# Kernel optimization log

Hardware: AMD Instinct MI355X
Metric: run time of the kernel (lower is better)

Reference implementation:

```python
import jax, jax.numpy as jnp
import numpy as np

T, HID, H, HKV, D = 4096, 2048, 16, 2, 128
EPS = 1e-6


def setup_inputs() -> dict:
    key = jax.random.key(0)
    ks = jax.random.split(key, 5)
    hidden_states = jax.random.normal(ks[0], (T, HID), dtype=jnp.float32)
    # rope angles: build realistic cos/sin from positions and inv-freqs
    inv_freq = 1.0 / (10000.0 ** (jnp.arange(0, D, 2, dtype=jnp.float32) / D))
    ang = jnp.arange(T, dtype=jnp.float32)[:, None] * inv_freq[None, :]  # [T, D/2]
    ang = jnp.concatenate([ang, ang], axis=-1)  # [T, D]
    cos, sin = jnp.cos(ang), jnp.sin(ang)
    w_qkv = jax.random.normal(ks[1], (HID, (2 * H + 2 * HKV) * D), dtype=jnp.float32) * (HID ** -0.5)
    w_o = jax.random.normal(ks[2], (H * D, HID), dtype=jnp.float32) * ((H * D) ** -0.5)
    q_norm_w = jnp.ones((D,), dtype=jnp.float32)
    k_norm_w = jnp.ones((D,), dtype=jnp.float32)
    return {"hidden_states": hidden_states, "cos": cos, "sin": sin,
            "w_qkv": w_qkv, "w_o": w_o, "q_norm_w": q_norm_w, "k_norm_w": k_norm_w}


def _rms_norm(x, w):
    var = jnp.mean(x * x, axis=-1, keepdims=True)
    return x * jax.lax.rsqrt(var + EPS) * w


def _rotate_half(x):
    x1, x2 = x[..., : D // 2], x[..., D // 2:]
    return jnp.concatenate([-x2, x1], axis=-1)


def _rope(x, cos, sin):
    # x: [T, h, D]; cos/sin: [T, D]
    return x * cos[:, None, :] + _rotate_half(x) * sin[:, None, :]


def reference(hidden_states, cos, sin, w_qkv, w_o, q_norm_w, k_norm_w):
    qkv = hidden_states @ w_qkv  # [T, (2H+2HKV)*D]
    q_sz, kv_sz = 2 * H * D, HKV * D
    # packed query+gate: view as [T, H, 2D], first half query, second half gate
    qg = qkv[:, :q_sz].reshape(T, H, 2 * D)
    q, gate = qg[..., :D], qg[..., D:]
    k = qkv[:, q_sz:q_sz + kv_sz].reshape(T, HKV, D)
    v = qkv[:, q_sz + kv_sz:].reshape(T, HKV, D)
    q = _rms_norm(q, q_norm_w)
    k = _rms_norm(k, k_norm_w)
    q = _rope(q, cos, sin)
    k = _rope(k, cos, sin)
    # GQA: expand kv heads to H
    rep = H // HKV
    k = jnp.repeat(k, rep, axis=1)  # [T, H, D]
    v = jnp.repeat(v, rep, axis=1)
    scale = D ** -0.5
    scores = jnp.einsum('thd,shd->hts', q, k) * scale  # [H, T, T]
    causal = jnp.tril(jnp.ones((T, T), dtype=bool))
    scores = jnp.where(causal[None], scores, jnp.finfo(scores.dtype).min)
    probs = jax.nn.softmax(scores, axis=-1)
    attn = jnp.einsum('hts,shd->thd', probs, v)  # [T, H, D]
    out = attn.reshape(T, H * D) * jax.nn.sigmoid(gate.reshape(T, H * D))
    return out @ w_o
```

## Files before the change

kernel.cpp:

```cpp
#include <hip/hip_runtime.h>
#include <hip/hip_bf16.h>
#include <math.h>


namespace {
constexpr int kT   = 4096;
constexpr int kHid = 2048;
constexpr int kH   = 16;
constexpr int kHkv = 2;
constexpr int kD   = 128;
constexpr int kNqkv = (2 * kH + 2 * kHkv) * kD;
constexpr int kQsz  = 2 * kH * kD;
constexpr int kRowU = kNqkv * 2;
constexpr float kEps = 1e-6f;
constexpr float kScale = 0.08838834764831845f;
}

typedef __attribute__((ext_vector_type(8))) short short8;
typedef __attribute__((ext_vector_type(4))) float floatx4;

__device__ inline unsigned short f2bf(float x) {
  unsigned u = __float_as_uint(x);
  u = (u + 0x7fffu + ((u >> 16) & 1u)) >> 16;
  return (unsigned short)u;
}

__device__ inline void gload_lds16(const void* g, void* l) {
  typedef const __attribute__((address_space(1))) unsigned GQ;
  typedef __attribute__((address_space(3))) unsigned LQ;
  __builtin_amdgcn_global_load_lds((GQ*)g, (LQ*)l, 16, 0, 0);
}

__global__ __launch_bounds__(256)
void prep_inputs(const float* __restrict__ hs, unsigned short* __restrict__ hsb,
                 const float* __restrict__ wqkv, unsigned short* __restrict__ wt) {
  __shared__ float t[32][33];
  const int b = blockIdx.x;
  if (b < 8192) {
    long i = ((long)b * 256 + threadIdx.x) * 4;
    float4 v = *(const float4*)(hs + i);
    unsigned long long p = (unsigned long long)f2bf(v.x) |
                           ((unsigned long long)f2bf(v.y) << 16) |
                           ((unsigned long long)f2bf(v.z) << 32) |
                           ((unsigned long long)f2bf(v.w) << 48);
    *(unsigned long long*)(hsb + i) = p;
    return;
  }
  const int b2 = b - 8192;
  const int bx = (b2 % 144) * 32;
  const int by = (b2 / 144) * 32;
  const int x = threadIdx.x & 31, y = threadIdx.x >> 5;
#pragma unroll
  for (int j = 0; j < 4; ++j)
    t[y * 4 + j][x] = wqkv[(long)(by + y * 4 + j) * kNqkv + bx + x];
  __syncthreads();
#pragma unroll
  for (int j = 0; j < 4; ++j)
    wt[(long)(bx + y * 4 + j) * kHid + by + x] = f2bf(t[x][y * 4 + j]);
}

__global__ __launch_bounds__(256)
void gemm_bf16(const unsigned short* __restrict__ A,
               const unsigned short* __restrict__ Bt, float* __restrict__ C,
               int M, int N, int K) {
  __shared__ __align__(16) unsigned short As[128 * 64];
  __shared__ __align__(16) unsigned short Bs[128 * 64];
  const int tid = threadIdx.x;
  const int lane = tid & 63;
  const int w = tid >> 6;
  const int wr = w >> 1, wc = w & 1;
  const int n = lane & 15;
  const int quad = lane >> 4;

  int bx = blockIdx.x, by = blockIdx.y;
  const int nbx = gridDim.x, nby = gridDim.y;
  if (nbx == 32 && ((nbx * nby) & 7) == 0) {
    int lin = bx + nbx * by;
    int xcd = lin & 7, s = lin >> 3;
    bx = 4 * xcd + (s & 3);
    by = s >> 2;
  }
  const long bm = (long)bx * 128, bn = (long)by * 128;

  floatx4 acc[4][4];
  floatx4 zero = {0.f, 0.f, 0.f, 0.f};
#pragma unroll
  for (int a = 0; a < 4; ++a)
#pragma unroll
    for (int b = 0; b < 4; ++b) acc[a][b] = zero;

  for (int k0 = 0; k0 < K; k0 += 64) {
    __syncthreads();
#pragma unroll
    for (int it = 0; it < 4; ++it) {
      int ci = it * 256 + tid;
      int r = ci >> 3, c = ci & 7;
      int cg = c ^ (r & 7);
      gload_lds16(A + (bm + r) * (long)K + k0 + cg * 8, As + (it * 256 + w * 64) * 8);
      gload_lds16(Bt + (bn + r) * (long)K + k0 + cg * 8, Bs + (it * 256 + w * 64) * 8);
    }
    __syncthreads();

#pragma unroll
    for (int ks = 0; ks < 2; ++ks) {
      short8 af[4], bf[4];
#pragma unroll
      for (int a = 0; a < 4; ++a) {
        int m = wr * 64 + a * 16 + n;
        af[a] = *(const short8*)(As + m * 64 + ((4 * ks + quad) ^ (m & 7)) * 8);
      }
#pragma unroll
      for (int b = 0; b < 4; ++b) {
        int nn = wc * 64 + b * 16 + n;
        bf[b] = *(const short8*)(Bs + nn * 64 + ((4 * ks + quad) ^ (nn & 7)) * 8);
      }
#pragma unroll
      for (int a = 0; a < 4; ++a)
#pragma unroll
        for (int b = 0; b < 4; ++b)
          acc[a][b] = __builtin_amdgcn_mfma_f32_16x16x32_bf16(af[a], bf[b], acc[a][b], 0, 0, 0);
    }
  }
#pragma unroll
  for (int a = 0; a < 4; ++a)
#pragma unroll
    for (int b = 0; b < 4; ++b)
#pragma unroll
      for (int r = 0; r < 4; ++r)
        C[(bm + wr * 64 + a * 16 + quad * 4 + r) * (long)N + bn + wc * 64 + b * 16 + n] =
            acc[a][b][r];
}

__global__ __launch_bounds__(256)
void vt_rope(float* qkv, unsigned short* __restrict__ VtG,
             const float* __restrict__ cosb, const float* __restrict__ sinb,
             const float* __restrict__ qw, const float* __restrict__ kw,
             const float* __restrict__ wo, unsigned short* __restrict__ woT) {
  __shared__ float t[32][33];
  const int b = blockIdx.x;
  if (b < 1024) {
    const int t0 = (b & 127) * 32;
    const int c0 = (b >> 7) * 32;
    const int x = threadIdx.x & 31, y = threadIdx.x >> 5;
#pragma unroll
    for (int j = 0; j < 4; ++j)
      t[y * 4 + j][x] = qkv[(long)(t0 + y * 4 + j) * kNqkv + 4352 + c0 + x];
    __syncthreads();
#pragma unroll
    for (int j = 0; j < 4; ++j)
      VtG[(long)(c0 + y * 4 + j) * kT + t0 + x] = f2bf(t[x][y * 4 + j]);
    return;
  }
  if (b >= 3328) {
    const int b3 = b - 3328;
    const int bx = (b3 & 63) * 32;
    const int by = (b3 >> 6) * 32;
    const int x = threadIdx.x & 31, y = threadIdx.x >> 5;
#pragma unroll
    for (int j = 0; j < 4; ++j)
      t[y * 4 + j][x] = wo[(long)(by + y * 4 + j) * kHid + bx + x];
    __syncthreads();
#pragma unroll
    for (int j = 0; j < 4; ++j)
      woT[(long)(bx + y * 4 + j) * kHid + by + x] = f2bf(t[x][y * 4 + j]);
    return;
  }
  unsigned short* qkvu = (unsigned short*)qkv;
  const int lane = threadIdx.x & 63;
  const int wslot = (b - 1024) * 4 + (threadIdx.x >> 6);
  const int nslots = 2304 * 4;
  for (int task = wslot; task < kT * 18; task += nslots) {
    const int tt = task / 18;
    const int h = task % 18;
    const bool isq = (h < kH);
    const long base = (long)tt * kNqkv + (isq ? h * 2 * kD : kQsz + (h - kH) * kD);
    float xlo = qkv[base + lane];
    float xhi = qkv[base + 64 + lane];
    float v = xlo * xlo + xhi * xhi;
#pragma unroll
    for (int off = 1; off < 64; off <<= 1) v += __shfl_xor(v, off, 64);
    float rms = rsqrtf(v * (1.0f / kD) + kEps);
    const float* wv = isq ? qw : kw;
    float nlo = xlo * rms * wv[lane];
    float nhi = xhi * rms * wv[64 + lane];
    float clo = cosb[tt * kD + lane], chi = cosb[tt * kD + 64 + lane];
    float slo = sinb[tt * kD + lane], shi = sinb[tt * kD + 64 + lane];
    float rlo = nlo * clo - nhi * slo;
    float rhi = nhi * chi + nlo * shi;
    if (isq) {
      float glo = qkv[base + kD + lane];
      float ghi = qkv[base + kD + 64 + lane];
      qkv[base + kD + lane] = 1.0f / (1.0f + __expf(-glo));
      qkv[base + kD + 64 + lane] = 1.0f / (1.0f + __expf(-ghi));
      qkvu[(long)tt * kRowU + 512 * h + lane] = f2bf(rlo);
      qkvu[(long)tt * kRowU + 512 * h + 64 + lane] = f2bf(rhi);
    } else {
      qkvu[(long)tt * kRowU + 8192 + 256 * (h - kH) + lane] = f2bf(rlo);
      qkvu[(long)tt * kRowU + 8192 + 256 * (h - kH) + 64 + lane] = f2bf(rhi);
    }
  }
}

__global__ __launch_bounds__(256)
void flash_attn_mfma(const unsigned short* qkvu, const float* qkvf,
                     const unsigned short* VtG, unsigned short* __restrict__ og) {
  __shared__ __align__(16) unsigned short Ks[64 * 128];
  __shared__ __align__(16) unsigned short Vt[128 * 64];
  __shared__ __align__(16) unsigned short Ps[128 * 64];

  const int tid = threadIdx.x;
  const int lane = tid & 63;
  const int w = tid >> 6;
  const int n = lane & 15;
  const int quad = lane >> 4;
  const int g = blockIdx.x;
  const int h = g & 15;
  const int bm = 31 - (g >> 4);
  const int hk = h >> 3;
  const int q0 = bm * 128;

  short8 qf[2][4];
#pragma unroll
  for (int mt = 0; mt < 2; ++mt) {
    const unsigned short* qrow =
        qkvu + (long)(q0 + 32 * w + 16 * mt + n) * kRowU + 512 * h;
#pragma unroll
    for (int ks = 0; ks < 4; ++ks)
      qf[mt][ks] = *(const short8*)(qrow + 32 * ks + 8 * quad);
  }
  short8 lfrag;
  {
    short o = (n == 0) ? (short)0x3F80 : (short)0;
    lfrag = (short8){o, o, o, o, o, o, o, o};
  }

  floatx4 O[2][8];
  floatx4 Ol[2];
  floatx4 zero = {0.f, 0.f, 0.f, 0.f};
#pragma unroll
  for (int mt = 0; mt < 2; ++mt) {
    Ol[mt] = zero;
#pragma unroll
    for (int dt = 0; dt < 8; ++dt) O[mt][dt] = zero;
  }

  const int kn_end = 2 * bm + 1;
  for (int kn = 0; kn <= kn_end; ++kn) {
    __syncthreads();
#pragma unroll
    for (int it = 0; it < 4; ++it) {
      int pc = (w * 4 + it) * 64 + lane;
      int r = pc >> 4, c = pc & 15;
      int lc = c ^ (r & 15);
      gload_lds16(qkvu + (long)(kn * 64 + r) * kRowU + 8192 + 256 * hk + 8 * lc,
                  Ks + (w * 4 + it) * 512);
    }
#pragma unroll
    for (int it = 0; it < 4; ++it) {
      int pc = (w * 4 + it) * 64 + lane;
      int d = pc >> 3, c = pc & 7;
      int lc = c ^ (d & 7);
      gload_lds16(VtG + (long)hk * (128 * kT) + (long)d * kT + kn * 64 + 8 * lc,
                  Vt + (w * 4 + it) * 512);
    }
    __syncthreads();

    floatx4 S[2][4];
#pragma unroll
    for (int mt = 0; mt < 2; ++mt)
#pragma unroll
      for (int ct = 0; ct < 4; ++ct) S[mt][ct] = zero;
#pragma unroll
    for (int ks = 0; ks < 4; ++ks) {
#pragma unroll
      for (int ct = 0; ct < 4; ++ct) {
        int row = 16 * ct + n;
        short8 kf = *(const short8*)(Ks + row * 128 + ((4 * ks + quad) ^ n) * 8);
        S[0][ct] = __builtin_amdgcn_mfma_f32_16x16x32_bf16(qf[0][ks], kf, S[0][ct], 0, 0, 0);
        S[1][ct] = __builtin_amdgcn_mfma_f32_16x16x32_bf16(qf[1][ks], kf, S[1][ct], 0, 0, 0);
      }
    }

    const bool needmask = (kn >= 2 * bm);
    const int jbase = (kn - 2 * bm) * 64;
    const int hi = n >> 3, lo = n & 7;
#pragma unroll
    for (int mt = 0; mt < 2; ++mt) {
#pragma unroll
      for (int r = 0; r < 4; ++r) {
        int prow = 32 * w + 16 * mt + quad * 4 + r;
        float p0 = __expf(S[mt][0][r] * kScale);
        float p1 = __expf(S[mt][1][r] * kScale);
        float p2 = __expf(S[mt][2][r] * kScale);
        float p3 = __expf(S[mt][3][r] * kScale);
        if (needmask) {
          if (jbase + n > prow) p0 = 0.f;
          if (jbase + 16 + n > prow) p1 = 0.f;
          if (jbase + 32 + n > prow) p2 = 0.f;
          if (jbase + 48 + n > prow) p3 = 0.f;
        }
        int sw = prow & 7;
        Ps[prow * 64 + (((0 + hi) ^ sw) << 3) + lo] = f2bf(p0);
        Ps[prow * 64 + (((2 + hi) ^ sw) << 3) + lo] = f2bf(p1);
        Ps[prow * 64 + (((4 + hi) ^ sw) << 3) + lo] = f2bf(p2);
        Ps[prow * 64 + (((6 + hi) ^ sw) << 3) + lo] = f2bf(p3);
      }
    }
    __asm__ volatile("s_waitcnt lgkmcnt(0)" ::: "memory");

#pragma unroll
    for (int ks = 0; ks < 2; ++ks) {
      int r0 = 32 * w + n, r1 = 32 * w + 16 + n;
      short8 pf0 = *(const short8*)(Ps + r0 * 64 + (((4 * ks + quad) ^ (r0 & 7)) << 3));
      short8 pf1 = *(const short8*)(Ps + r1 * 64 + (((4 * ks + quad) ^ (r1 & 7)) << 3));
      Ol[0] = __builtin_amdgcn_mfma_f32_16x16x32_bf16(pf0, lfrag, Ol[0], 0, 0, 0);
      Ol[1] = __builtin_amdgcn_mfma_f32_16x16x32_bf16(pf1, lfrag, Ol[1], 0, 0, 0);
#pragma unroll
      for (int dt = 0; dt < 8; ++dt) {
        int d = 16 * dt + n;
        short8 vf = *(const short8*)(Vt + d * 64 + (((4 * ks + quad) ^ (d & 7)) << 3));
        O[0][dt] = __builtin_amdgcn_mfma_f32_16x16x32_bf16(pf0, vf, O[0][dt], 0, 0, 0);
        O[1][dt] = __builtin_amdgcn_mfma_f32_16x16x32_bf16(pf1, vf, O[1][dt], 0, 0, 0);
      }
    }
  }

#pragma unroll
  for (int mt = 0; mt < 2; ++mt) {
#pragma unroll
    for (int r = 0; r < 4; ++r) {
      float l = __shfl(Ol[mt][r], quad << 4, 64);
      float inv = 1.0f / l;
      int row = q0 + 32 * w + 16 * mt + quad * 4 + r;
#pragma unroll
      for (int dt = 0; dt < 8; ++dt) {
        int col = 16 * dt + n;
        float gte = qkvf[(long)row * kNqkv + 256 * h + 128 + col];
        og[(long)row * kHid + 128 * h + col] = f2bf(O[mt][dt][r] * inv * gte);
      }
    }
  }
}

extern "C" void kernel_launch(void* const* d_in, const int* in_sizes, int n_in,
                              void* d_out, int out_size, void* d_ws, size_t ws_size,
                              hipStream_t stream) {
  (void)in_sizes; (void)n_in; (void)out_size; (void)ws_size;
  const float* hs   = (const float*)d_in[0];
  const float* cosb = (const float*)d_in[1];
  const float* sinb = (const float*)d_in[2];
  const float* wqkv = (const float*)d_in[3];
  const float* wo   = (const float*)d_in[4];
  const float* qw   = (const float*)d_in[5];
  const float* kw   = (const float*)d_in[6];
  float* out = (float*)d_out;

  char* ws = (char*)d_ws;
  float* qkv = (float*)ws;
  unsigned short* hsb = (unsigned short*)(ws + 75497472);
  unsigned short* og  = hsb;
  unsigned short* wt  = (unsigned short*)(ws + 92274688);
  unsigned short* VtG = wt;
  unsigned short* woT = (unsigned short*)(ws + 92274688 + 8388608);

  prep_inputs<<<dim3(17408), 256, 0, stream>>>(hs, hsb, wqkv, wt);
  gemm_bf16<<<dim3(kT / 128, kNqkv / 128), 256, 0, stream>>>(hsb, wt, qkv, kT, kNqkv, kHid);
  vt_rope<<<dim3(7424), 256, 0, stream>>>(qkv, VtG, cosb, sinb, qw, kw, wo, woT);
  flash_attn_mfma<<<dim3(kT / 128 * kH), 256, 0, stream>>>((const unsigned short*)qkv, qkv, VtG, og);
  gemm_bf16<<<dim3(kT / 128, kHid / 128), 256, 0, stream>>>(og, woT, out, kT, kHid, kHid);
}
```

Baseline: 470.8 us.

## Fuse QK RMSNorm, RoPE and gate sigmoid into the QKV GEMM epilogue

```diff
diff --git a/kernel.cpp b/kernel.cpp
--- a/kernel.cpp
+++ b/kernel.cpp
@@ -62,7 +62,9 @@
 __global__ __launch_bounds__(256)
 void gemm_bf16(const unsigned short* __restrict__ A,
                const unsigned short* __restrict__ Bt, float* __restrict__ C,
-               int M, int N, int K) {
+               int M, int N, int K, int mode,
+               const float* __restrict__ cosb, const float* __restrict__ sinb,
+               const float* __restrict__ qw, const float* __restrict__ kw) {
   __shared__ __align__(16) unsigned short As[128 * 64];
   __shared__ __align__(16) unsigned short Bs[128 * 64];
   const int tid = threadIdx.x;
@@ -111,7 +113,7 @@
       }
 #pragma unroll
       for (int b = 0; b < 4; ++b) {
-        int nn = wc * 64 + b * 16 + n;
+        int nn = ((b & 1) << 6) + ((b >> 1) << 5) + wc * 16 + n;
         bf[b] = *(const short8*)(Bs + nn * 64 + ((4 * ks + quad) ^ (nn & 7)) * 8);
       }
 #pragma unroll
@@ -121,27 +123,86 @@
           acc[a][b] = __builtin_amdgcn_mfma_f32_16x16x32_bf16(af[a], bf[b], acc[a][b], 0, 0, 0);
     }
   }
+
+  const bool qkTile = (mode == 1) && (bn < 4352) && ((bn >= 4096) || !(bn & 128));
+  const bool gateTile = (mode == 1) && (bn < 4096) && (bn & 128);
+  if (qkTile) {
+    __syncthreads();
+    float* sums = (float*)As;
+#pragma unroll
+    for (int a = 0; a < 4; ++a)
+#pragma unroll
+      for (int r = 0; r < 4; ++r) {
+        float s = 0.f;
+#pragma unroll
+        for (int b = 0; b < 4; ++b) { float v = acc[a][b][r]; s += v * v; }
+#pragma unroll
+        for (int off = 1; off < 16; off <<= 1) s += __shfl_xor(s, off, 64);
+        if (n == 0) sums[wc * 128 + wr * 64 + a * 16 + quad * 4 + r] = s;
+      }
+    __syncthreads();
+    const float* wv = (bn < 4096) ? qw : kw;
+    const int hdOff = (bn < 4096) ? (int)(bn >> 8) * 512
+                                  : 8192 + (int)((bn - 4096) >> 7) * 256;
+    unsigned short* qkvu = (unsigned short*)C;
+#pragma unroll
+    for (int a = 0; a < 4; ++a)
+#pragma unroll
+      for (int r = 0; r < 4; ++r) {
+        int lr = wr * 64 + a * 16 + quad * 4 + r;
+        long t = bm + lr;
+        float rms = rsqrtf((sums[lr] + sums[128 + lr]) * (1.0f / kD) + kEps);
+        float nv[4];
+#pragma unroll
+        for (int b = 0; b < 4; ++b) {
+          int d = ((b & 1) << 6) + ((b >> 1) << 5) + wc * 16 + n;
+          nv[b] = acc[a][b][r] * rms * wv[d];
+        }
+#pragma unroll
+        for (int b = 0; b < 4; ++b) {
+          int d = ((b & 1) << 6) + ((b >> 1) << 5) + wc * 16 + n;
+          float cv = cosb[t * kD + d], sv = sinb[t * kD + d];
+          float p = nv[b ^ 1];
+          float o = (b & 1) ? (nv[b] * cv + p * sv) : (nv[b] * cv - p * sv);
+          qkvu[t * (long)kRowU + hdOff + d] = f2bf(o);
+        }
+      }
+    return;
+  }
+  if (gateTile) {
+#pragma unroll
+    for (int a = 0; a < 4; ++a)
+#pragma unroll
+      for (int b = 0; b < 4; ++b) {
+        int d = ((b & 1) << 6) + ((b >> 1) << 5) + wc * 16 + n;
+#pragma unroll
+        for (int r = 0; r < 4; ++r)
+          C[(bm + wr * 64 + a * 16 + quad * 4 + r) * (long)N + bn + d] =
+              1.0f / (1.0f + __expf(-acc[a][b][r]));
+      }
+    return;
+  }
 #pragma unroll
   for (int a = 0; a < 4; ++a)
 #pragma unroll
-    for (int b = 0; b < 4; ++b)
+    for (int b = 0; b < 4; ++b) {
+      int d = ((b & 1) << 6) + ((b >> 1) << 5) + wc * 16 + n;
 #pragma unroll
       for (int r = 0; r < 4; ++r)
-        C[(bm + wr * 64 + a * 16 + quad * 4 + r) * (long)N + bn + wc * 64 + b * 16 + n] =
+        C[(bm + wr * 64 + a * 16 + quad * 4 + r) * (long)N + bn + d] =
             acc[a][b][r];
+    }
 }
 
 __global__ __launch_bounds__(256)
-void vt_rope(float* qkv, unsigned short* __restrict__ VtG,
-             const float* __restrict__ cosb, const float* __restrict__ sinb,
-             const float* __restrict__ qw, const float* __restrict__ kw,
-             const float* __restrict__ wo, unsigned short* __restrict__ woT) {
+void vt_wo(const float* __restrict__ qkv, unsigned short* __restrict__ VtG,
+           const float* __restrict__ wo, unsigned short* __restrict__ woT) {
   __shared__ float t[32][33];
   const int b = blockIdx.x;
+  const int x = threadIdx.x & 31, y = threadIdx.x >> 5;
   if (b < 1024) {
     const int t0 = (b & 127) * 32;
     const int c0 = (b >> 7) * 32;
-    const int x = threadIdx.x & 31, y = threadIdx.x >> 5;
 #pragma unroll
     for (int j = 0; j < 4; ++j)
       t[y * 4 + j][x] = qkv[(long)(t0 + y * 4 + j) * kNqkv + 4352 + c0 + x];
@@ -151,54 +212,16 @@
       VtG[(long)(c0 + y * 4 + j) * kT + t0 + x] = f2bf(t[x][y * 4 + j]);
     return;
   }
-  if (b >= 3328) {
-    const int b3 = b - 3328;
-    const int bx = (b3 & 63) * 32;
-    const int by = (b3 >> 6) * 32;
-    const int x = threadIdx.x & 31, y = threadIdx.x >> 5;
-#pragma unroll
-    for (int j = 0; j < 4; ++j)
-      t[y * 4 + j][x] = wo[(long)(by + y * 4 + j) * kHid + bx + x];
-    __syncthreads();
-#pragma unroll
-    for (int j = 0; j < 4; ++j)
-      woT[(long)(bx + y * 4 + j) * kHid + by + x] = f2bf(t[x][y * 4 + j]);
-    return;
-  }
-  unsigned short* qkvu = (unsigned short*)qkv;
-  const int lane = threadIdx.x & 63;
-  const int wslot = (b - 1024) * 4 + (threadIdx.x >> 6);
-  const int nslots = 2304 * 4;
-  for (int task = wslot; task < kT * 18; task += nslots) {
-    const int tt = task / 18;
-    const int h = task % 18;
-    const bool isq = (h < kH);
-    const long base = (long)tt * kNqkv + (isq ? h * 2 * kD : kQsz + (h - kH) * kD);
-    float xlo = qkv[base + lane];
-    float xhi = qkv[base + 64 + lane];
-    float v = xlo * xlo + xhi * xhi;
-#pragma unroll
-    for (int off = 1; off < 64; off <<= 1) v += __shfl_xor(v, off, 64);
-    float rms = rsqrtf(v * (1.0f / kD) + kEps);
-    const float* wv = isq ? qw : kw;
-    float nlo = xlo * rms * wv[lane];
-    float nhi = xhi * rms * wv[64 + lane];
-    float clo = cosb[tt * kD + lane], chi = cosb[tt * kD + 64 + lane];
-    float slo = sinb[tt * kD + lane], shi = sinb[tt * kD + 64 + lane];
-    float rlo = nlo * clo - nhi * slo;
-    float rhi = nhi * chi + nlo * shi;
-    if (isq) {
-      float glo = qkv[base + kD + lane];
-      float ghi = qkv[base + kD + 64 + lane];
-      qkv[base + kD + lane] = 1.0f / (1.0f + __expf(-glo));
-      qkv[base + kD + 64 + lane] = 1.0f / (1.0f + __expf(-ghi));
-      qkvu[(long)tt * kRowU + 512 * h + lane] = f2bf(rlo);
-      qkvu[(long)tt * kRowU + 512 * h + 64 + lane] = f2bf(rhi);
-    } else {
-      qkvu[(long)tt * kRowU + 8192 + 256 * (h - kH) + lane] = f2bf(rlo);
-      qkvu[(long)tt * kRowU + 8192 + 256 * (h - kH) + 64 + lane] = f2bf(rhi);
-    }
-  }
+  const int b3 = b - 1024;
+  const int bx = (b3 & 63) * 32;
+  const int by = (b3 >> 6) * 32;
+#pragma unroll
+  for (int j = 0; j < 4; ++j)
+    t[y * 4 + j][x] = wo[(long)(by + y * 4 + j) * kHid + bx + x];
+  __syncthreads();
+#pragma unroll
+  for (int j = 0; j < 4; ++j)
+    woT[(long)(bx + y * 4 + j) * kHid + by + x] = f2bf(t[x][y * 4 + j]);
 }
 
 __global__ __launch_bounds__(256)
@@ -364,8 +387,10 @@
   unsigned short* woT = (unsigned short*)(ws + 92274688 + 8388608);
 
   prep_inputs<<<dim3(17408), 256, 0, stream>>>(hs, hsb, wqkv, wt);
-  gemm_bf16<<<dim3(kT / 128, kNqkv / 128), 256, 0, stream>>>(hsb, wt, qkv, kT, kNqkv, kHid);
-  vt_rope<<<dim3(7424), 256, 0, stream>>>(qkv, VtG, cosb, sinb, qw, kw, wo, woT);
+  gemm_bf16<<<dim3(kT / 128, kNqkv / 128), 256, 0, stream>>>(
+      hsb, wt, qkv, kT, kNqkv, kHid, 1, cosb, sinb, qw, kw);
+  vt_wo<<<dim3(5120), 256, 0, stream>>>(qkv, VtG, wo, woT);
   flash_attn_mfma<<<dim3(kT / 128 * kH), 256, 0, stream>>>((const unsigned short*)qkv, qkv, VtG, og);
-  gemm_bf16<<<dim3(kT / 128, kHid / 128), 256, 0, stream>>>(og, woT, out, kT, kHid, kHid);
-}
+  gemm_bf16<<<dim3(kT / 128, kHid / 128), 256, 0, stream>>>(
+      og, woT, out, kT, kHid, kHid, 0, nullptr, nullptr, nullptr, nullptr);
+}
```

New measurement: 455.7 us. 3.2% less time.
